# Kernel optimization log

Hardware: AMD Instinct MI355X
Metric: run time of the kernel (lower is better)

## Reference

```python
import jax, jax.numpy as jnp
import numpy as np

B, N, K, CIN, COUT, H = 4, 2048, 32, 16, 32, 32
EPS = 1e-5


def setup_inputs() -> dict:
    key = jax.random.key(0)
    ks = jax.random.split(key, 6)
    s = 0.1
    return dict(
        xyz=jax.random.uniform(ks[0], (B, N, 3), dtype=jnp.float32),
        points=jax.random.normal(ks[1], (B, N, CIN), dtype=jnp.float32),
        W1=jax.random.normal(ks[2], (3, H), dtype=jnp.float32) * s,
        b1=jnp.zeros((H,), jnp.float32),
        g1=jnp.ones((H,), jnp.float32),
        be1=jnp.zeros((H,), jnp.float32),
        W2=jax.random.normal(ks[3], (H, H), dtype=jnp.float32) * s,
        b2=jnp.zeros((H,), jnp.float32),
        g2=jnp.ones((H,), jnp.float32),
        be2=jnp.zeros((H,), jnp.float32),
        W3=jax.random.normal(ks[4], (H, CIN * COUT), dtype=jnp.float32) * s,
        b3=jnp.zeros((CIN * COUT,), jnp.float32),
        gbn=jnp.ones((COUT,), jnp.float32),
        bbn=jnp.zeros((COUT,), jnp.float32),
    )


def _bn(h, g, b):
    # BatchNorm1d training-mode math: biased batch stats over axis 0
    return g * (h - h.mean(0)) / jnp.sqrt(h.var(0) + EPS) + b


def reference(xyz, points, W1, b1, g1, be1, W2, b2, g2, be2, W3, b3, gbn, bbn):
    # KNN: squared distances (B,N,N)
    sq = jnp.sum(xyz * xyz, -1)
    dist = -2.0 * jnp.einsum('bmc,bnc->bmn', xyz, xyz) + sq[:, :, None] + sq[:, None, :]
    _, idx = jax.lax.top_k(-dist, K)  # (B,N,K) nearest neighbors

    gather = jax.vmap(lambda p, i: p[i])  # (N,C),(N,K)->(N,K,C), vmapped over B
    grouped_xyz = gather(xyz, idx)                      # (B,N,K,3)
    rel = grouped_xyz - xyz[:, :, None, :]              # (B,N,K,3)
    grouped_pts = gather(points, idx)                   # (B,N,K,CIN)

    # weight net on relative coords
    h = rel.reshape(-1, 3)
    h = _bn(jax.nn.relu(h @ W1 + b1), g1, be1)
    h = _bn(jax.nn.relu(h @ W2 + b2), g2, be2)
    w = (h @ W3 + b3).reshape(B, N, K, CIN, COUT)       # (B,N,K,CIN,COUT)

    # weighted sum over C_in, then max over neighbors
    out = jnp.einsum('bnkc,bnkco->bnko', grouped_pts, w)  # (B,N,K,COUT)
    out = out.max(axis=2)                                 # (B,N,COUT)

    # final BatchNorm1d over (B,N) per channel
    m = out.mean((0, 1))
    v = out.var((0, 1))
    return gbn * (out - m) / jnp.sqrt(v + EPS) + bbn
```

## Files before the change

### kernel.cpp

```cpp
#include <hip/hip_runtime.h>

#define B_ 4
#define N_ 2048
#define K_ 32
#define CIN_ 16
#define COUT_ 32
#define H_ 32
#define R_ (B_*N_*K_)
#define EPS_ 1e-5f
#define INVR_ (1.0f/(float)R_)
#define INVBN_ (1.0f/(float)(B_*N_))
#define LISTCAP 160
#define NSH 16

typedef __attribute__((ext_vector_type(8)))  _Float16 f16x8;
typedef __attribute__((ext_vector_type(2)))  __fp16   hw16x2;
typedef __attribute__((ext_vector_type(2)))  _Float16 f16x2;
typedef __attribute__((ext_vector_type(16))) float    f32x16;

__device__ __forceinline__ float dot3f(float ax,float ay,float az,float bx,float by,float bz){
    return fmaf(az,bz, fmaf(ay,by, ax*bx));
}
__device__ __forceinline__ unsigned int pk2(float a, float b){
    union { hw16x2 v; unsigned int u; } c;
    c.v = __builtin_amdgcn_cvt_pkrtz(a, b);
    return c.u;
}
__device__ __forceinline__ unsigned int pkmul(unsigned int a, unsigned int b){
    union { unsigned int u; f16x2 v; } x, y, r;
    x.u = a; y.u = b; r.v = x.v * y.v; return r.u;
}
__device__ __forceinline__ float shsum(const float* __restrict__ p, int k){
    float s = 0.f;
    #pragma unroll
    for (int i = 0; i < NSH; ++i) s += p[i*32 + k];
    return s;
}

__global__ __launch_bounds__(256) void k_prep0(const float* __restrict__ xyz, const float* __restrict__ points,
                                               float4* __restrict__ xs4g, unsigned int* __restrict__ pf16,
                                               float* __restrict__ st){
    int flat = blockIdx.x*256 + threadIdx.x;
    if (flat < 8192){
        float x = xyz[3*flat], y = xyz[3*flat+1], z = xyz[3*flat+2];
        xs4g[flat] = make_float4(x, y, z, dot3f(x,y,z,x,y,z));
    } else {
        int p = flat - 8192;
        pf16[p] = pk2(points[2*p], points[2*p+1]);
    }
    if (blockIdx.x == 0){
        for (int j = threadIdx.x; j < 1280; j += 256) st[j] = 0.f;
    }
}

__global__ __launch_bounds__(256,5) void k_knn(const float4* __restrict__ xs4g,
                                               const float* __restrict__ W1, const float* __restrict__ b1,
                                               int* __restrict__ idx_out,
                                               float* __restrict__ s1sh, float* __restrict__ q1sh,
                                               unsigned int* __restrict__ h1f){
    __shared__ unsigned int hist[4][512][2];
    __shared__ unsigned long long lst[4][LISTCAP];
    __shared__ int kidx[4][K_];

    const int tid  = threadIdx.x;
    const int w    = tid >> 6;
    const int lane = tid & 63;
    const int half = lane >> 5;
    const int b    = blockIdx.x >> 9;
    const int q    = ((blockIdx.x & 511) << 2) + w;
    const int bN   = b * N_;
    unsigned int* hw = &hist[w][0][0];

    const uint4 z4 = make_uint4(0,0,0,0);
    uint4* h4 = (uint4*)hw;
    #pragma unroll
    for (int i = 0; i < 4; ++i) h4[i*64 + lane] = z4;

    const float4 qp = xs4g[bN + q];
    const float qx = qp.x, qy = qp.y, qz = qp.z, sqq = qp.w;

    unsigned int fv[32];
    #pragma unroll
    for (int j = 0; j < 32; ++j){
        int c = j*64 + lane;
        float4 pt = xs4g[bN + c];
        float d = fmaf(-2.0f, dot3f(qx,qy,qz, pt.x,pt.y,pt.z), sqq) + pt.w;
        fv[j] = __float_as_uint(d);
        unsigned int u1 = __float_as_uint(d + 1.0f);
        unsigned int key = (u1 <= 0x3F800000u) ? 0u : ((u1 - 0x3F800000u) >> 15);
        key = key > 511u ? 511u : key;
        atomicAdd(&hw[key*2 + (lane & 1)], 1u);
    }

    unsigned int g[8];
    #pragma unroll
    for (int t = 0; t < 4; ++t){
        uint4 h = ((const uint4*)hw)[lane*4 + t];
        g[2*t]   = h.x + h.y;
        g[2*t+1] = h.z + h.w;
    }
    unsigned int gs = 0;
    #pragma unroll
    for (int t = 0; t < 8; ++t) gs += g[t];
    unsigned int cum = gs;
    #pragma unroll
    for (int off = 1; off < 64; off <<= 1){
        unsigned int v = __shfl_up(cum, off);
        if (lane >= off) cum += v;
    }
    unsigned long long bal = __ballot(cum >= (unsigned)K_);
    int L = __ffsll(bal) - 1;
    unsigned int run = __shfl(cum, L) - __shfl(gs, L);
    int Bsel = 8*L + 7;
    {
        unsigned int c = run; bool fnd = false;
        #pragma unroll
        for (int t = 0; t < 8; ++t){
            unsigned int ht = __shfl(g[t], L, 64);
            if (!fnd && c + ht >= (unsigned)K_){ Bsel = 8*L + t; fnd = true; }
            c += ht;
        }
    }
    const float Tedge = __uint_as_float(0x3F800000u + ((unsigned)(Bsel + 1) << 15));
    const bool allin = (Bsel == 511);

    const unsigned long long mlt = (lane == 63) ? ~0ull >> 1 : (1ull << lane) - 1ull;
    unsigned int cnt = 0;
    #pragma unroll
    for (int j = 0; j < 32; ++j){
        float f1 = __uint_as_float(fv[j]) + 1.0f;
        bool surv = (f1 < Tedge) || allin;
        unsigned long long sb = __ballot(surv);
        unsigned int pos = cnt + (unsigned int)__popcll(sb & mlt);
        if (surv && pos < (unsigned)LISTCAP)
            lst[w][pos] = ((unsigned long long)fv[j] << 32) | (unsigned int)(j*64 + lane);
        cnt += (unsigned int)__popcll(sb);
    }
    int m = (int)cnt; if (m > LISTCAP) m = LISTCAP;

    int* outp = idx_out + ((size_t)bN + q) * K_;
    for (int i = lane; i < m; i += 64){
        unsigned long long my = lst[w][i];
        int rank = 0;
        for (int jj = 0; jj < m; ++jj)
            rank += (lst[w][jj] < my) ? 1 : 0;
        if (rank < K_){
            int id = (int)(unsigned int)(my & 0xFFFFFFFFull);
            outp[rank] = id;
            kidx[w][rank] = id;
        }
    }

    {
        const int ch = lane & 31;
        float w1a = W1[ch], w1b = W1[H_+ch], w1c = W1[2*H_+ch], b1c = b1[ch];
        float s = 0.f, qq = 0.f;
        #pragma unroll
        for (int r = 0; r < 16; ++r){
            int idr = kidx[w][half*16 + r];
            float4 pn = xs4g[bN + idr];
            float rx = pn.x - qx, ry = pn.y - qy, rz = pn.z - qz;
            float h = fmaxf(fmaf(rx, w1a, fmaf(ry, w1b, fmaf(rz, w1c, b1c))), 0.0f);
            s += h; qq = fmaf(h, h, qq);
        }
        s  += __shfl_xor(s, 32, 64);
        qq += __shfl_xor(qq, 32, 64);
        if (lane < 32){
            int sh = (blockIdx.x & (NSH-1)) * 32 + ch;
            atomicAdd(&s1sh[sh], s);
            atomicAdd(&q1sh[sh], qq);
        }
    }

    {
        const int id = kidx[w][lane & 31];
        float4 pn = xs4g[bN + id];
        float rx = pn.x - qx, ry = pn.y - qy, rz = pn.z - qz;
        uint4* dst = (uint4*)h1f + (size_t)(bN + q)*128 + lane;
        const int c0 = half*8;
        #pragma unroll
        for (int sblk = 0; sblk < 2; ++sblk){
            const int cb = sblk*16 + c0;
            const float4 wa0 = *(const float4*)(W1 + cb);
            const float4 wa1 = *(const float4*)(W1 + cb + 4);
            const float4 wb0 = *(const float4*)(W1 + H_ + cb);
            const float4 wb1 = *(const float4*)(W1 + H_ + cb + 4);
            const float4 wc0 = *(const float4*)(W1 + 2*H_ + cb);
            const float4 wc1 = *(const float4*)(W1 + 2*H_ + cb + 4);
            const float4 bv0 = *(const float4*)(b1 + cb);
            const float4 bv1 = *(const float4*)(b1 + cb + 4);
            float h0 = fmaxf(fmaf(rx, wa0.x, fmaf(ry, wb0.x, fmaf(rz, wc0.x, bv0.x))), 0.0f);
            float h1v= fmaxf(fmaf(rx, wa0.y, fmaf(ry, wb0.y, fmaf(rz, wc0.y, bv0.y))), 0.0f);
            float h2v= fmaxf(fmaf(rx, wa0.z, fmaf(ry, wb0.z, fmaf(rz, wc0.z, bv0.z))), 0.0f);
            float h3 = fmaxf(fmaf(rx, wa0.w, fmaf(ry, wb0.w, fmaf(rz, wc0.w, bv0.w))), 0.0f);
            float h4 = fmaxf(fmaf(rx, wa1.x, fmaf(ry, wb1.x, fmaf(rz, wc1.x, bv1.x))), 0.0f);
            float h5 = fmaxf(fmaf(rx, wa1.y, fmaf(ry, wb1.y, fmaf(rz, wc1.y, bv1.y))), 0.0f);
            float h6 = fmaxf(fmaf(rx, wa1.z, fmaf(ry, wb1.z, fmaf(rz, wc1.z, bv1.z))), 0.0f);
            float h7 = fmaxf(fmaf(rx, wa1.w, fmaf(ry, wb1.w, fmaf(rz, wc1.w, bv1.w))), 0.0f);
            uint4 o;
            o.x = pk2(h0, h1v); o.y = pk2(h2v, h3); o.z = pk2(h4, h5); o.w = pk2(h6, h7);
            dst[sblk*64] = o;
        }
    }
}

__device__ __forceinline__ void build_l2(const float* __restrict__ s1s, const float* __restrict__ q1s,
                                         const float* __restrict__ g1, const float* __restrict__ be1,
                                         const float* __restrict__ W2, const float* __restrict__ b2,
                                         float* a1L, float* bb1L, unsigned int* W2L, float* b2pL,
                                         int tid){
    if (tid < H_){
        float s = shsum(s1s, tid), qq = shsum(q1s, tid);
        float mm = s*INVR_, vv = qq*INVR_ - mm*mm;
        float aa = g1[tid] / sqrtf(vv + EPS_);
        a1L[tid]  = aa;
        bb1L[tid] = fmaf(-aa, mm, be1[tid]);
    }
    __syncthreads();
    #pragma unroll
    for (int e = 0; e < 2; ++e){
        int d = tid*2 + e;
        int jj = d & 3, ln = (d >> 2) & 63, s = d >> 8;
        int col = ln & 31;
        int k0 = s*16 + ((ln >> 5) << 3) + 2*jj;
        W2L[d] = pk2(a1L[k0]*W2[k0*H_ + col], a1L[k0+1]*W2[(k0+1)*H_ + col]);
    }
    if (tid < H_){
        float acc = b2[tid];
        #pragma unroll 4
        for (int h = 0; h < H_; ++h) acc = fmaf(bb1L[h], W2[h*H_ + tid], acc);
        b2pL[tid] = acc;
    }
}

__global__ __launch_bounds__(256,4) void k_h2stats(const uint4* __restrict__ h1f,
                                                   const float* __restrict__ s1s, const float* __restrict__ q1s,
                                                   const float* __restrict__ g1, const float* __restrict__ be1,
                                                   const float* __restrict__ W2, const float* __restrict__ b2,
                                                   float* gsum, float* gsq){
    __shared__ float redS[H_], redQ[H_];
    __shared__ float a1L[H_], bb1L[H_], b2pL[H_];
    __shared__ unsigned int W2L[512];
    const int tid = threadIdx.x, lane = tid & 63, w = tid >> 6;
    const int m = lane & 31;
    if (tid < H_){ redS[tid] = 0.f; redQ[tid] = 0.f; }
    build_l2(s1s, q1s, g1, be1, W2, b2, a1L, bb1L, W2L, b2pL, tid);
    __syncthreads();

    union { uint4 u4; f16x8 v; } Bf0, Bf1;
    Bf0.u4 = ((const uint4*)W2L)[lane];
    Bf1.u4 = ((const uint4*)W2L)[64 + lane];
    float b2c = b2pL[m];
    const int blk0 = blockIdx.x*16 + w*4;

    float s = 0.f, q = 0.f;
    #pragma unroll
    for (int t = 0; t < 4; ++t){
        union { uint4 u4; f16x8 v; } a0, a1f;
        a0.u4  = h1f[(size_t)(blk0 + t)*128 + lane];
        a1f.u4 = h1f[(size_t)(blk0 + t)*128 + 64 + lane];
        f32x16 acc;
        #pragma unroll
        for (int i = 0; i < 16; ++i) acc[i] = b2c;
        acc = __builtin_amdgcn_mfma_f32_32x32x16_f16(a0.v,  Bf0.v, acc, 0, 0, 0);
        acc = __builtin_amdgcn_mfma_f32_32x32x16_f16(a1f.v, Bf1.v, acc, 0, 0, 0);
        #pragma unroll
        for (int i = 0; i < 16; ++i){
            float v = fmaxf(acc[i], 0.0f);
            s += v; q = fmaf(v, v, q);
        }
    }
    s += __shfl_xor(s, 32, 64);
    q += __shfl_xor(q, 32, 64);
    if (lane < 32){ atomicAdd(&redS[m], s); atomicAdd(&redQ[m], q); }
    __syncthreads();
    if (tid < H_){ atomicAdd(&gsum[tid], redS[tid]); atomicAdd(&gsq[tid], redQ[tid]); }
}

#define PHASEA(T, H2P, GSEL) do { \
    union { uint4 u4; f16x8 v; } B0f, B1f; \
    B0f.u4 = h1f[(size_t)(blk0 + (T))*128 + lane]; \
    B1f.u4 = h1f[(size_t)(blk0 + (T))*128 + 64 + lane]; \
    int row = rB + (T)*32 + m; \
    int bb_ = row >> 16; \
    int idr = idx[row]; \
    const uint4* gpp = (const uint4*)(pf16 + ((size_t)bb_*N_ + idr)*8); \
    uint4 ga = gpp[0], gb = gpp[1]; \
    GSEL[0] = half ? gb.x : ga.x; \
    GSEL[1] = half ? gb.y : ga.y; \
    GSEL[2] = half ? gb.z : ga.z; \
    GSEL[3] = half ? gb.w : ga.w; \
    f32x16 c2; \
    _Pragma("unroll") \
    for (int i = 0; i < 16; ++i) c2[i] = b2v[i]; \
    c2 = __builtin_amdgcn_mfma_f32_32x32x16_f16(A0.v, B0f.v, c2, 0, 0, 0); \
    c2 = __builtin_amdgcn_mfma_f32_32x32x16_f16(A1.v, B1f.v, c2, 0, 0, 0); \
    _Pragma("unroll") \
    for (int p = 0; p < 8; ++p){ \
        float v0 = fmaxf(c2[2*p],   0.0f); \
        float v1 = fmaxf(c2[2*p+1], 0.0f); \
        unsigned int ow = pk2(v0, v1); \
        unsigned int ot = __shfl_xor(ow, 32, 64); \
        int a = p >> 1, bb = p & 1; \
        H2P[4*a + bb]     = half ? ot : ow; \
        H2P[4*a + 2 + bb] = half ? ow : ot; \
    } \
} while(0)

#define REDST(ACC, T) do { \
    float v = ACC[0]; \
    _Pragma("unroll") \
    for (int i = 1; i < 16; ++i) v = fmaxf(v, ACC[i]); \
    v = fmaxf(v, __shfl_xor(v, 32, 64)); \
    if (lane < 32){ \
        int g = blk0 + (T); \
        out_pre[(size_t)g*COUT_ + m] = v; \
        atomicAdd(&redS[m], v); \
        atomicAdd(&redQ[m], v*v); \
    } \
} while(0)

__global__ __launch_bounds__(256,4) void k_out(const uint4* __restrict__ h1f, const int* __restrict__ idx,
                                               const float* __restrict__ s1s, const float* __restrict__ q1s,
                                               const float* __restrict__ g1, const float* __restrict__ be1,
                                               const float* __restrict__ W2, const float* __restrict__ b2,
                                               const float* __restrict__ s2, const float* __restrict__ q2,
                                               const float* __restrict__ g2, const float* __restrict__ be2,
                                               const float* __restrict__ W3, const float* __restrict__ b3,
                                               const unsigned int* __restrict__ pf16,
                                               float* __restrict__ out_pre, float* gsum, float* gsq){
    __shared__ uint4 Wls[2112];
    __shared__ float redS[COUT_], redQ[COUT_];
    __shared__ float a1L[H_], bb1L[H_], b2pL[H_], aa2L[H_], bb2L[H_];
    __shared__ unsigned int W2L[512];
    const int tid = threadIdx.x, lane = tid & 63, w = tid >> 6;
    const int half = lane >> 5, m = lane & 31;
    if (tid < COUT_){
        redS[tid] = 0.f; redQ[tid] = 0.f;
        float mm = s2[tid]*INVR_, vv = q2[tid]*INVR_ - mm*mm;
        float aa = g2[tid] / sqrtf(vv + EPS_);
        aa2L[tid] = aa;
        bb2L[tid] = fmaf(-aa, mm, be2[tid]);
    }
    build_l2(s1s, q1s, g1, be1, W2, b2, a1L, bb1L, W2L, b2pL, tid);
    {
        int jj = tid & 3, ln = tid >> 2;
        int col = ln & 31, c0 = ((ln >> 5) << 3) + 2*jj;
        unsigned int* WlsD = (unsigned int*)Wls;
        #pragma unroll 4
        for (int i = 0; i < 32; ++i){
            float a = aa2L[i];
            WlsD[i*256 + tid] = pk2(a*W3[i*512 + c0*COUT_ + col], a*W3[i*512 + (c0+1)*COUT_ + col]);
        }
        float v0 = b3[c0*COUT_ + col], v1 = b3[(c0+1)*COUT_ + col];
        #pragma unroll 4
        for (int h = 0; h < H_; ++h){
            v0 = fmaf(bb2L[h], W3[h*512 + c0*COUT_ + col], v0);
            v1 = fmaf(bb2L[h], W3[h*512 + (c0+1)*COUT_ + col], v1);
        }
        WlsD[32*256 + tid] = pk2(v0, v1);
    }
    __syncthreads();

    const int rB = blockIdx.x*256 + w*64;
    const int blk0 = blockIdx.x*8 + w*2;

    union { uint4 u4; f16x8 v; } A0, A1;
    A0.u4 = ((const uint4*)W2L)[lane];
    A1.u4 = ((const uint4*)W2L)[64 + lane];
    float b2v[16];
    #pragma unroll
    for (int i = 0; i < 16; ++i) b2v[i] = b2pL[(i&3) + 8*(i>>2) + 4*half];

    unsigned int h2p0[16], h2p1[16];
    unsigned int gsel0[4], gsel1[4];
    PHASEA(0, h2p0, gsel0);
    PHASEA(1, h2p1, gsel1);

    f32x16 acc0, acc1;
    #pragma unroll
    for (int i = 0; i < 16; ++i){ acc0[i] = 0.f; acc1[i] = 0.f; }
    #pragma unroll
    for (int kb = 0; kb < 32; ++kb){
        union { uint4 u4; f16x8 v; } bf; bf.u4 = Wls[kb*64 + lane];
        const unsigned int sel = (kb & 1) ? 0x03020302u : 0x01000100u;
        unsigned int hr0 = h2p0[kb >> 1];
        unsigned int hd0 = __builtin_amdgcn_perm(hr0, hr0, sel);
        union { unsigned int u[4]; f16x8 v; } af;
        #pragma unroll
        for (int jj = 0; jj < 4; ++jj) af.u[jj] = pkmul(hd0, gsel0[jj]);
        acc0 = __builtin_amdgcn_mfma_f32_32x32x16_f16(af.v, bf.v, acc0, 0, 0, 0);
        unsigned int hr1 = h2p1[kb >> 1];
        unsigned int hd1 = __builtin_amdgcn_perm(hr1, hr1, sel);
        #pragma unroll
        for (int jj = 0; jj < 4; ++jj) af.u[jj] = pkmul(hd1, gsel1[jj]);
        acc1 = __builtin_amdgcn_mfma_f32_32x32x16_f16(af.v, bf.v, acc1, 0, 0, 0);
    }
    {
        union { uint4 u4; f16x8 v; } bf; bf.u4 = Wls[32*64 + lane];
        union { unsigned int u[4]; f16x8 v; } af;
        #pragma unroll
        for (int jj = 0; jj < 4; ++jj) af.u[jj] = gsel0[jj];
        acc0 = __builtin_amdgcn_mfma_f32_32x32x16_f16(af.v, bf.v, acc0, 0, 0, 0);
        #pragma unroll
        for (int jj = 0; jj < 4; ++jj) af.u[jj] = gsel1[jj];
        acc1 = __builtin_amdgcn_mfma_f32_32x32x16_f16(af.v, bf.v, acc1, 0, 0, 0);
    }

    REDST(acc0, 0);
    REDST(acc1, 1);

    __syncthreads();
    if (tid < COUT_){ atomicAdd(&gsum[tid], redS[tid]); atomicAdd(&gsq[tid], redQ[tid]); }
}

__global__ __launch_bounds__(256) void k_bn(const float4* __restrict__ out_pre4,
                                            const float* __restrict__ s3, const float* __restrict__ q3,
                                            const float* __restrict__ gbn, const float* __restrict__ bbn,
                                            float4* __restrict__ out4){
    int i = blockIdx.x*256 + threadIdx.x;
    int o = (i*4) & (COUT_-1);
    float4 v = out_pre4[i];
    float4 r;
    {
        float mm = s3[o]*INVBN_;   float vv = q3[o]*INVBN_   - mm*mm;
        float aa = gbn[o]/sqrtf(vv+EPS_);   r.x = fmaf(aa, v.x, fmaf(-aa, mm, bbn[o]));
    }
    {
        float mm = s3[o+1]*INVBN_; float vv = q3[o+1]*INVBN_ - mm*mm;
        float aa = gbn[o+1]/sqrtf(vv+EPS_); r.y = fmaf(aa, v.y, fmaf(-aa, mm, bbn[o+1]));
    }
    {
        float mm = s3[o+2]*INVBN_; float vv = q3[o+2]*INVBN_ - mm*mm;
        float aa = gbn[o+2]/sqrtf(vv+EPS_); r.z = fmaf(aa, v.z, fmaf(-aa, mm, bbn[o+2]));
    }
    {
        float mm = s3[o+3]*INVBN_; float vv = q3[o+3]*INVBN_ - mm*mm;
        float aa = gbn[o+3]/sqrtf(vv+EPS_); r.w = fmaf(aa, v.w, fmaf(-aa, mm, bbn[o+3]));
    }
    out4[i] = r;
}

extern "C" void kernel_launch(void* const* d_in, const int* in_sizes, int n_in,
                              void* d_out, int out_size, void* d_ws, size_t ws_size,
                              hipStream_t stream){
    const float* xyz    = (const float*)d_in[0];
    const float* points = (const float*)d_in[1];
    const float* W1  = (const float*)d_in[2];
    const float* b1  = (const float*)d_in[3];
    const float* g1  = (const float*)d_in[4];
    const float* be1 = (const float*)d_in[5];
    const float* W2  = (const float*)d_in[6];
    const float* b2  = (const float*)d_in[7];
    const float* g2  = (const float*)d_in[8];
    const float* be2 = (const float*)d_in[9];
    const float* W3  = (const float*)d_in[10];
    const float* b3  = (const float*)d_in[11];
    const float* gbn = (const float*)d_in[12];
    const float* bbn = (const float*)d_in[13];
    float* out = (float*)d_out;

    char* base = (char*)d_ws;
    int*            idx     = (int*)(base + 0);
    float*          out_pre = (float*)(base + 1048576);
    unsigned int*   pf16    = (unsigned int*)(base + 2097152);
    float*          st      = (float*)(base + 2395264);
    float4*         xs4g    = (float4*)(base + 2400384);
    unsigned int*   h1f     = (unsigned int*)(base + 4194304);
    float *s1s=st, *q1s=st+512, *s2=st+1024, *q2=st+1056, *s3=st+1088, *q3=st+1120;

    hipLaunchKernelGGL(k_prep0,   dim3(288),      dim3(256), 0, stream, xyz, points, xs4g, pf16, st);
    hipLaunchKernelGGL(k_knn,     dim3(B_*N_/4),  dim3(256), 0, stream, xs4g, W1, b1, idx, s1s, q1s, h1f);
    hipLaunchKernelGGL(k_h2stats, dim3(R_/512),   dim3(256), 0, stream, (const uint4*)h1f,
                       s1s, q1s, g1, be1, W2, b2, s2, q2);
    hipLaunchKernelGGL(k_out,     dim3(R_/256),   dim3(256), 0, stream, (const uint4*)h1f, idx,
                       s1s, q1s, g1, be1, W2, b2, s2, q2, g2, be2, W3, b3, pf16, out_pre, s3, q3);
    hipLaunchKernelGGL(k_bn,      dim3(256),      dim3(256), 0, stream, (const float4*)out_pre, s3, q3,
                       gbn, bbn, (float4*)out);
}
```

Baseline: 169.8 us.

## Split each KNN query across two wavefronts with shared histogram and list

Each query point in the KNN kernel is now handled by two wavefronts instead of one. They share an LDS histogram and candidate list, with block-level barriers and a per-wave survivor count used to compute list offsets. This halves per-wave register state (16 distances instead of 32), shrinks LDS per block, and raises the occupancy hint to 7, doubling the grid size. The cost is extra __syncthreads, an additional ballot pass to count survivors, and coordination overhead between the waves.

```diff
diff --git a/kernel.cpp b/kernel.cpp
--- a/kernel.cpp
+++ b/kernel.cpp
@@ -53,36 +53,43 @@
     }
 }
 
-__global__ __launch_bounds__(256,5) void k_knn(const float4* __restrict__ xs4g,
+__global__ __launch_bounds__(256,7) void k_knn(const float4* __restrict__ xs4g,
                                                const float* __restrict__ W1, const float* __restrict__ b1,
                                                int* __restrict__ idx_out,
                                                float* __restrict__ s1sh, float* __restrict__ q1sh,
                                                unsigned int* __restrict__ h1f){
-    __shared__ unsigned int hist[4][512][2];
-    __shared__ unsigned long long lst[4][LISTCAP];
-    __shared__ int kidx[4][K_];
+    __shared__ unsigned int hist[2][512][2];
+    __shared__ unsigned long long lst[2][LISTCAP];
+    __shared__ int kidx[2][K_];
+    __shared__ unsigned int cntW[2][2];
 
     const int tid  = threadIdx.x;
     const int w    = tid >> 6;
     const int lane = tid & 63;
     const int half = lane >> 5;
-    const int b    = blockIdx.x >> 9;
-    const int q    = ((blockIdx.x & 511) << 2) + w;
+    const int p    = w >> 1;
+    const int ws   = w & 1;
+    const int qg   = blockIdx.x*2 + p;
+    const int b    = qg >> 11;
+    const int q    = qg & (N_-1);
     const int bN   = b * N_;
-    unsigned int* hw = &hist[w][0][0];
-
-    const uint4 z4 = make_uint4(0,0,0,0);
-    uint4* h4 = (uint4*)hw;
-    #pragma unroll
-    for (int i = 0; i < 4; ++i) h4[i*64 + lane] = z4;
+    unsigned int* hw = &hist[p][0][0];
+
+    {
+        const uint4 z4 = make_uint4(0,0,0,0);
+        uint4* h4 = (uint4*)hw;
+        int t2 = ws*64 + lane;
+        h4[t2] = z4; h4[128 + t2] = z4;
+    }
+    __syncthreads();
 
     const float4 qp = xs4g[bN + q];
     const float qx = qp.x, qy = qp.y, qz = qp.z, sqq = qp.w;
 
-    unsigned int fv[32];
-    #pragma unroll
-    for (int j = 0; j < 32; ++j){
-        int c = j*64 + lane;
+    unsigned int fv[16];
+    #pragma unroll
+    for (int j = 0; j < 16; ++j){
+        int c = j*128 + ws*64 + lane;
         float4 pt = xs4g[bN + c];
         float d = fmaf(-2.0f, dot3f(qx,qy,qz, pt.x,pt.y,pt.z), sqq) + pt.w;
         fv[j] = __float_as_uint(d);
@@ -91,6 +98,7 @@
         key = key > 511u ? 511u : key;
         atomicAdd(&hw[key*2 + (lane & 1)], 1u);
     }
+    __syncthreads();
 
     unsigned int g[8];
     #pragma unroll
@@ -124,40 +132,52 @@
     const float Tedge = __uint_as_float(0x3F800000u + ((unsigned)(Bsel + 1) << 15));
     const bool allin = (Bsel == 511);
 
+    unsigned int myc = 0;
+    #pragma unroll
+    for (int j = 0; j < 16; ++j){
+        float f1 = __uint_as_float(fv[j]) + 1.0f;
+        bool surv = (f1 < Tedge) || allin;
+        myc += (unsigned int)__popcll(__ballot(surv));
+    }
+    if (lane == 0) cntW[p][ws] = myc;
+    __syncthreads();
+
     const unsigned long long mlt = (lane == 63) ? ~0ull >> 1 : (1ull << lane) - 1ull;
-    unsigned int cnt = 0;
-    #pragma unroll
-    for (int j = 0; j < 32; ++j){
+    unsigned int cnt = ws ? cntW[p][0] : 0u;
+    #pragma unroll
+    for (int j = 0; j < 16; ++j){
         float f1 = __uint_as_float(fv[j]) + 1.0f;
         bool surv = (f1 < Tedge) || allin;
         unsigned long long sb = __ballot(surv);
         unsigned int pos = cnt + (unsigned int)__popcll(sb & mlt);
         if (surv && pos < (unsigned)LISTCAP)
-            lst[w][pos] = ((unsigned long long)fv[j] << 32) | (unsigned int)(j*64 + lane);
+            lst[p][pos] = ((unsigned long long)fv[j] << 32) | (unsigned int)(j*128 + ws*64 + lane);
         cnt += (unsigned int)__popcll(sb);
     }
-    int m = (int)cnt; if (m > LISTCAP) m = LISTCAP;
+    __syncthreads();
+    int m = (int)(cntW[p][0] + cntW[p][1]); if (m > LISTCAP) m = LISTCAP;
 
     int* outp = idx_out + ((size_t)bN + q) * K_;
-    for (int i = lane; i < m; i += 64){
-        unsigned long long my = lst[w][i];
+    for (int i = ws*64 + lane; i < m; i += 128){
+        unsigned long long my = lst[p][i];
         int rank = 0;
         for (int jj = 0; jj < m; ++jj)
-            rank += (lst[w][jj] < my) ? 1 : 0;
+            rank += (lst[p][jj] < my) ? 1 : 0;
         if (rank < K_){
             int id = (int)(unsigned int)(my & 0xFFFFFFFFull);
             outp[rank] = id;
-            kidx[w][rank] = id;
-        }
-    }
+            kidx[p][rank] = id;
+        }
+    }
+    __syncthreads();
 
     {
         const int ch = lane & 31;
         float w1a = W1[ch], w1b = W1[H_+ch], w1c = W1[2*H_+ch], b1c = b1[ch];
         float s = 0.f, qq = 0.f;
         #pragma unroll
-        for (int r = 0; r < 16; ++r){
-            int idr = kidx[w][half*16 + r];
+        for (int r = 0; r < 8; ++r){
+            int idr = kidx[p][ws*16 + half*8 + r];
             float4 pn = xs4g[bN + idr];
             float rx = pn.x - qx, ry = pn.y - qy, rz = pn.z - qz;
             float h = fmaxf(fmaf(rx, w1a, fmaf(ry, w1b, fmaf(rz, w1c, b1c))), 0.0f);
@@ -173,34 +193,30 @@
     }
 
     {
-        const int id = kidx[w][lane & 31];
+        const int id = kidx[p][lane & 31];
         float4 pn = xs4g[bN + id];
         float rx = pn.x - qx, ry = pn.y - qy, rz = pn.z - qz;
-        uint4* dst = (uint4*)h1f + (size_t)(bN + q)*128 + lane;
-        const int c0 = half*8;
-        #pragma unroll
-        for (int sblk = 0; sblk < 2; ++sblk){
-            const int cb = sblk*16 + c0;
-            const float4 wa0 = *(const float4*)(W1 + cb);
-            const float4 wa1 = *(const float4*)(W1 + cb + 4);
-            const float4 wb0 = *(const float4*)(W1 + H_ + cb);
-            const float4 wb1 = *(const float4*)(W1 + H_ + cb + 4);
-            const float4 wc0 = *(const float4*)(W1 + 2*H_ + cb);
-            const float4 wc1 = *(const float4*)(W1 + 2*H_ + cb + 4);
-            const float4 bv0 = *(const float4*)(b1 + cb);
-            const float4 bv1 = *(const float4*)(b1 + cb + 4);
-            float h0 = fmaxf(fmaf(rx, wa0.x, fmaf(ry, wb0.x, fmaf(rz, wc0.x, bv0.x))), 0.0f);
-            float h1v= fmaxf(fmaf(rx, wa0.y, fmaf(ry, wb0.y, fmaf(rz, wc0.y, bv0.y))), 0.0f);
-            float h2v= fmaxf(fmaf(rx, wa0.z, fmaf(ry, wb0.z, fmaf(rz, wc0.z, bv0.z))), 0.0f);
-            float h3 = fmaxf(fmaf(rx, wa0.w, fmaf(ry, wb0.w, fmaf(rz, wc0.w, bv0.w))), 0.0f);
-            float h4 = fmaxf(fmaf(rx, wa1.x, fmaf(ry, wb1.x, fmaf(rz, wc1.x, bv1.x))), 0.0f);
-            float h5 = fmaxf(fmaf(rx, wa1.y, fmaf(ry, wb1.y, fmaf(rz, wc1.y, bv1.y))), 0.0f);
-            float h6 = fmaxf(fmaf(rx, wa1.z, fmaf(ry, wb1.z, fmaf(rz, wc1.z, bv1.z))), 0.0f);
-            float h7 = fmaxf(fmaf(rx, wa1.w, fmaf(ry, wb1.w, fmaf(rz, wc1.w, bv1.w))), 0.0f);
-            uint4 o;
-            o.x = pk2(h0, h1v); o.y = pk2(h2v, h3); o.z = pk2(h4, h5); o.w = pk2(h6, h7);
-            dst[sblk*64] = o;
-        }
+        uint4* dst = (uint4*)h1f + (size_t)(bN + q)*128 + ws*64 + lane;
+        const int cb = ws*16 + half*8;
+        const float4 wa0 = *(const float4*)(W1 + cb);
+        const float4 wa1 = *(const float4*)(W1 + cb + 4);
+        const float4 wb0 = *(const float4*)(W1 + H_ + cb);
+        const float4 wb1 = *(const float4*)(W1 + H_ + cb + 4);
+        const float4 wc0 = *(const float4*)(W1 + 2*H_ + cb);
+        const float4 wc1 = *(const float4*)(W1 + 2*H_ + cb + 4);
+        const float4 bv0 = *(const float4*)(b1 + cb);
+        const float4 bv1 = *(const float4*)(b1 + cb + 4);
+        float h0 = fmaxf(fmaf(rx, wa0.x, fmaf(ry, wb0.x, fmaf(rz, wc0.x, bv0.x))), 0.0f);
+        float h1v= fmaxf(fmaf(rx, wa0.y, fmaf(ry, wb0.y, fmaf(rz, wc0.y, bv0.y))), 0.0f);
+        float h2v= fmaxf(fmaf(rx, wa0.z, fmaf(ry, wb0.z, fmaf(rz, wc0.z, bv0.z))), 0.0f);
+        float h3 = fmaxf(fmaf(rx, wa0.w, fmaf(ry, wb0.w, fmaf(rz, wc0.w, bv0.w))), 0.0f);
+        float h4 = fmaxf(fmaf(rx, wa1.x, fmaf(ry, wb1.x, fmaf(rz, wc1.x, bv1.x))), 0.0f);
+        float h5 = fmaxf(fmaf(rx, wa1.y, fmaf(ry, wb1.y, fmaf(rz, wc1.y, bv1.y))), 0.0f);
+        float h6 = fmaxf(fmaf(rx, wa1.z, fmaf(ry, wb1.z, fmaf(rz, wc1.z, bv1.z))), 0.0f);
+        float h7 = fmaxf(fmaf(rx, wa1.w, fmaf(ry, wb1.w, fmaf(rz, wc1.w, bv1.w))), 0.0f);
+        uint4 o;
+        o.x = pk2(h0, h1v); o.y = pk2(h2v, h3); o.z = pk2(h4, h5); o.w = pk2(h6, h7);
+        *dst = o;
     }
 }
 
@@ -470,7 +486,7 @@
     float *s1s=st, *q1s=st+512, *s2=st+1024, *q2=st+1056, *s3=st+1088, *q3=st+1120;
 
     hipLaunchKernelGGL(k_prep0,   dim3(288),      dim3(256), 0, stream, xyz, points, xs4g, pf16, st);
-    hipLaunchKernelGGL(k_knn,     dim3(B_*N_/4),  dim3(256), 0, stream, xs4g, W1, b1, idx, s1s, q1s, h1f);
+    hipLaunchKernelGGL(k_knn,     dim3(B_*N_/2),  dim3(256), 0, stream, xs4g, W1, b1, idx, s1s, q1s, h1f);
     hipLaunchKernelGGL(k_h2stats, dim3(R_/512),   dim3(256), 0, stream, (const uint4*)h1f,
                        s1s, q1s, g1, be1, W2, b2, s2, q2);
     hipLaunchKernelGGL(k_out,     dim3(R_/256),   dim3(256), 0, stream, (const uint4*)h1f, idx,
```

Result: slower. 174.5 us (+2.8%).
